# Optimization experiments

Measured on AMD Instinct MI355X. Metric: run time of the kernel, lower is better.

## Reference

```python
import jax, jax.numpy as jnp
import numpy as np

DUNITS = 1024
ATT_DIM = 1024
EPROJ = 1024
T = 16384
SCALING = 2.0


def setup_inputs() -> dict:
    key = jax.random.key(0)
    ks = jax.random.split(key, 8)
    dec_z = jax.random.normal(ks[0], (1, DUNITS), dtype=jnp.float32)
    att_prev = jnp.zeros((1, T), dtype=jnp.float32)
    pre_compute_enc_h = jax.random.normal(ks[1], (1, T, ATT_DIM), dtype=jnp.float32)
    enc_h = jax.random.normal(ks[2], (1, T, EPROJ), dtype=jnp.float32)
    mask = jnp.zeros((1, T), dtype=jnp.float32)
    # learned params: mlp_dec Linear(dunits->att_dim), gvec Linear(att_dim->1)
    W_dec = jax.random.normal(ks[3], (DUNITS, ATT_DIM), dtype=jnp.float32) / np.sqrt(DUNITS)
    b_dec = jnp.zeros((ATT_DIM,), dtype=jnp.float32)
    w_gvec = jax.random.normal(ks[4], (ATT_DIM,), dtype=jnp.float32) / np.sqrt(ATT_DIM)
    b_gvec = jnp.zeros((), dtype=jnp.float32)
    return {
        "dec_z": dec_z,
        "att_prev": att_prev,
        "pre_compute_enc_h": pre_compute_enc_h,
        "enc_h": enc_h,
        "mask": mask,
        "W_dec": W_dec,
        "b_dec": b_dec,
        "w_gvec": w_gvec,
        "b_gvec": b_gvec,
    }


def reference(dec_z, att_prev, pre_compute_enc_h, enc_h, mask, W_dec, b_dec, w_gvec, b_gvec):
    # dec_z: [1, dunits] -> mlp_dec -> [1, 1, att_dim]
    dec_z_tiled = (dec_z @ W_dec + b_dec)[:, None, :]
    # gvec(tanh(pre + tile)).squeeze(2): [1, T]
    e = jnp.einsum("bta,a->bt", jnp.tanh(pre_compute_enc_h + dec_z_tiled), w_gvec) + b_gvec
    e = e + mask
    w = jax.nn.softmax(SCALING * e, axis=1)  # [1, T]
    c = jnp.einsum("bte,bt->be", enc_h, w)   # [1, eproj]
    return (c, w)
```

## Files before the change

### kernel.cpp

```cpp
#include <hip/hip_runtime.h>
#include <math.h>

#define TT   16384
#define ADIM 1024
#define NCH  2048
#define RPB  8
#define NCH2 128

__device__ __forceinline__ float ftanh(float x) {
    float e2 = __expf(2.0f * x);
    return 1.0f - 2.0f * __builtin_amdgcn_rcpf(e2 + 1.0f);
}

__device__ __forceinline__ float pdot(float4 p, float4 d, float4 g) {
    return ftanh(p.x + d.x) * g.x + ftanh(p.y + d.y) * g.y +
           ftanh(p.z + d.z) * g.z + ftanh(p.w + d.w) * g.w;
}

__global__ void k1_gemv_part(const float* __restrict__ z, const float* __restrict__ W,
                             float* __restrict__ part) {
    int b = blockIdx.x, tid = threadIdx.x;
    float4 acc = {0.f, 0.f, 0.f, 0.f};
#pragma unroll
    for (int i = 0; i < 4; ++i) {
        int d = b * 4 + i;
        float zv = z[d];
        float4 w4 = reinterpret_cast<const float4*>(W)[(size_t)d * 256 + tid];
        acc.x += zv * w4.x; acc.y += zv * w4.y; acc.z += zv * w4.z; acc.w += zv * w4.w;
    }
    reinterpret_cast<float4*>(part)[(size_t)b * 256 + tid] = acc;
}

__global__ void k2_gemv_red(const float* __restrict__ part, const float* __restrict__ bdec,
                            float* __restrict__ dp) {
    int b = blockIdx.x, tid = threadIdx.x;
    int lane = tid & 63, wv = tid >> 6;
    int rsub = lane >> 2;
    int colg = lane & 3;
    float4 acc = {0.f, 0.f, 0.f, 0.f};
#pragma unroll
    for (int i = 0; i < 4; ++i) {
        int row = i * 64 + wv * 16 + rsub;
        float4 v = reinterpret_cast<const float4*>(part)[(size_t)row * 256 + b * 4 + colg];
        acc.x += v.x; acc.y += v.y; acc.z += v.z; acc.w += v.w;
    }
#pragma unroll
    for (int off = 4; off <= 32; off <<= 1) {
        acc.x += __shfl_xor(acc.x, off, 64);
        acc.y += __shfl_xor(acc.y, off, 64);
        acc.z += __shfl_xor(acc.z, off, 64);
        acc.w += __shfl_xor(acc.w, off, 64);
    }
    __shared__ float4 lds[4][4];
    if (lane < 4) lds[wv][lane] = acc;
    __syncthreads();
    if (tid < 4) {
        float4 t = {0.f, 0.f, 0.f, 0.f};
#pragma unroll
        for (int w = 0; w < 4; ++w) {
            float4 v = lds[w][tid];
            t.x += v.x; t.y += v.y; t.z += v.z; t.w += v.w;
        }
        float4 bd = reinterpret_cast<const float4*>(bdec)[b * 4 + tid];
        t.x += bd.x; t.y += bd.y; t.z += bd.z; t.w += bd.w;
        reinterpret_cast<float4*>(dp)[b * 4 + tid] = t;
    }
}

__global__ void __launch_bounds__(256) k3_fused(
    const float* __restrict__ pre, const float* __restrict__ enc,
    const float* __restrict__ dp, const float* __restrict__ wg,
    const float* __restrict__ bgp, const float* __restrict__ mask,
    float* __restrict__ e_out, float* __restrict__ m_out,
    float* __restrict__ s_out, float* __restrict__ cpart) {
    int b = blockIdx.x, tid = threadIdx.x;
    int lane = tid & 63, wv = tid >> 6;
    int col = wv * 64 + lane;
    float4 d4 = reinterpret_cast<const float4*>(dp)[col];
    float4 g4 = reinterpret_cast<const float4*>(wg)[col];
    float bgv = bgp[0];
    int t0 = b * RPB;
    const float4* pb = reinterpret_cast<const float4*>(pre) + (size_t)t0 * 256 + col;
    const float4* eb = reinterpret_cast<const float4*>(enc) + (size_t)t0 * 256 + col;

    float4 pv[RPB], ev[RPB];
#pragma unroll
    for (int r = 0; r < RPB; ++r) pv[r] = pb[r * 256];
#pragma unroll
    for (int r = 0; r < RPB; ++r) ev[r] = eb[r * 256];

    float dt[RPB];
#pragma unroll
    for (int r = 0; r < RPB; ++r) dt[r] = pdot(pv[r], d4, g4);
#pragma unroll
    for (int r = 0; r < RPB; ++r) {
#pragma unroll
        for (int off = 32; off; off >>= 1) dt[r] += __shfl_xor(dt[r], off, 64);
    }
    __shared__ float sd[4][RPB];
    if (lane == 0) {
#pragma unroll
        for (int r = 0; r < RPB; ++r) sd[wv][r] = dt[r];
    }
    __syncthreads();
    float et[RPB];
#pragma unroll
    for (int r = 0; r < RPB; ++r)
        et[r] = 2.0f * (sd[0][r] + sd[1][r] + sd[2][r] + sd[3][r] + bgv + mask[t0 + r]);
    if (tid == 0) {
#pragma unroll
        for (int r = 0; r < RPB; ++r) e_out[t0 + r] = et[r];
    }

    float m = et[0];
#pragma unroll
    for (int r = 1; r < RPB; ++r) m = fmaxf(m, et[r]);
    float p[RPB], s = 0.f;
#pragma unroll
    for (int r = 0; r < RPB; ++r) { p[r] = __expf(et[r] - m); s += p[r]; }
    if (tid == 0) { m_out[b] = m; s_out[b] = s; }

    float4 ca = {0.f, 0.f, 0.f, 0.f};
#pragma unroll
    for (int r = 0; r < RPB; ++r) {
        ca.x += p[r] * ev[r].x; ca.y += p[r] * ev[r].y;
        ca.z += p[r] * ev[r].z; ca.w += p[r] * ev[r].w;
    }
    reinterpret_cast<float4*>(cpart)[(size_t)b * 256 + col] = ca;
}

__global__ void __launch_bounds__(256) k4_fold(
    const float* __restrict__ m_arr, const float* __restrict__ s_arr,
    const float* __restrict__ cpart, float* __restrict__ cpart2,
    float* __restrict__ msout) {
    int b = blockIdx.x, tid = threadIdx.x;
    int lane = tid & 63, wv = tid >> 6;
    __shared__ float redm[4], reds[4];
    float mloc = -3.0e38f;
#pragma unroll
    for (int i = 0; i < NCH / 256; ++i) mloc = fmaxf(mloc, m_arr[tid + i * 256]);
#pragma unroll
    for (int off = 32; off; off >>= 1) mloc = fmaxf(mloc, __shfl_xor(mloc, off, 64));
    if (lane == 0) redm[wv] = mloc;
    __syncthreads();
    float M = fmaxf(fmaxf(redm[0], redm[1]), fmaxf(redm[2], redm[3]));
    float4 acc = {0.f, 0.f, 0.f, 0.f};
#pragma unroll
    for (int i = 0; i < NCH / NCH2; ++i) {
        int r = b * (NCH / NCH2) + i;
        float scf = __expf(m_arr[r] - M);
        float4 v = reinterpret_cast<const float4*>(cpart)[(size_t)r * 256 + tid];
        acc.x += scf * v.x; acc.y += scf * v.y; acc.z += scf * v.z; acc.w += scf * v.w;
    }
    reinterpret_cast<float4*>(cpart2)[(size_t)b * 256 + tid] = acc;
    if (b == 0) {
        float sl = 0.f;
#pragma unroll
        for (int i = 0; i < NCH / 256; ++i)
            sl += s_arr[tid + i * 256] * __expf(m_arr[tid + i * 256] - M);
#pragma unroll
        for (int off = 32; off; off >>= 1) sl += __shfl_xor(sl, off, 64);
        if (lane == 0) reds[wv] = sl;
        __syncthreads();
        if (tid == 0) {
            float S = reds[0] + reds[1] + reds[2] + reds[3];
            msout[0] = M;
            msout[1] = 1.0f / S;
        }
    }
}

__global__ void __launch_bounds__(256) k5_final(
    const float* __restrict__ cpart2, const float* __restrict__ e,
    const float* __restrict__ ms, float* __restrict__ c_out,
    float* __restrict__ w_out) {
    int b = blockIdx.x, tid = threadIdx.x;
    float M = ms[0], invS = ms[1];
    if (b < 16) {
        int rs = tid >> 4;
        int cg = tid & 15;
        float4 acc = {0.f, 0.f, 0.f, 0.f};
#pragma unroll
        for (int i = 0; i < NCH2 / 16; ++i) {
            int r = rs * (NCH2 / 16) + i;
            float4 v = reinterpret_cast<const float4*>(cpart2)[(size_t)r * 256 + b * 16 + cg];
            acc.x += v.x; acc.y += v.y; acc.z += v.z; acc.w += v.w;
        }
        __shared__ float4 lds[16][16];
        lds[rs][cg] = acc;
        __syncthreads();
        if (tid < 16) {
            float4 t = {0.f, 0.f, 0.f, 0.f};
#pragma unroll
            for (int r = 0; r < 16; ++r) {
                float4 v = lds[r][tid];
                t.x += v.x; t.y += v.y; t.z += v.z; t.w += v.w;
            }
            t.x *= invS; t.y *= invS; t.z *= invS; t.w *= invS;
            reinterpret_cast<float4*>(c_out)[b * 16 + tid] = t;
        }
    } else {
        int base = (b - 16) * 256 + tid;
        float4 ev = reinterpret_cast<const float4*>(e)[base];
        float4 w;
        w.x = __expf(ev.x - M) * invS;
        w.y = __expf(ev.y - M) * invS;
        w.z = __expf(ev.z - M) * invS;
        w.w = __expf(ev.w - M) * invS;
        reinterpret_cast<float4*>(w_out)[base] = w;
    }
}

extern "C" void kernel_launch(void* const* d_in, const int* in_sizes, int n_in,
                              void* d_out, int out_size, void* d_ws, size_t ws_size,
                              hipStream_t stream) {
    const float* dec_z = (const float*)d_in[0];
    const float* pre   = (const float*)d_in[2];
    const float* enc   = (const float*)d_in[3];
    const float* mask  = (const float*)d_in[4];
    const float* W_dec = (const float*)d_in[5];
    const float* b_dec = (const float*)d_in[6];
    const float* wg    = (const float*)d_in[7];
    const float* bg    = (const float*)d_in[8];

    float* out   = (float*)d_out;
    float* c_out = out;
    float* w_out = out + ADIM;

    float* ws = (float*)d_ws;
    float* part   = ws;
    float* dp     = part + 256 * ADIM;
    float* e_sc   = dp + ADIM;
    float* m_arr  = e_sc + TT;
    float* s_arr  = m_arr + NCH;
    float* cpart  = s_arr + NCH;
    float* cpart2 = cpart + (size_t)NCH * ADIM;
    float* ms     = cpart2 + (size_t)NCH2 * ADIM;

    k1_gemv_part<<<256, 256, 0, stream>>>(dec_z, W_dec, part);
    k2_gemv_red<<<64, 256, 0, stream>>>(part, b_dec, dp);
    k3_fused<<<NCH, 256, 0, stream>>>(pre, enc, dp, wg, bg, mask,
                                      e_sc, m_arr, s_arr, cpart);
    k4_fold<<<NCH2, 256, 0, stream>>>(m_arr, s_arr, cpart, cpart2, ms);
    k5_final<<<32, 256, 0, stream>>>(cpart2, e_sc, ms, c_out, w_out);
}
```

Before: 39.85 us.

## Merge fold and final kernels, double rows per block in main pass

Halves the number of main-kernel blocks by processing 16 rows each and loads rows inline instead of prefetching all of them into registers. The separate fold kernel is removed: the final kernel has every block recompute the global max and sum and directly rescale-reduce all per-chunk partials. This removes one launch and the intermediate partial buffer round-trip. The trade-off is a longer serial reduction over 1024 partials in only 16 blocks and less memory-level parallelism in the main pass.

```diff
diff --git a/kernel.cpp b/kernel.cpp
--- a/kernel.cpp
+++ b/kernel.cpp
@@ -3,9 +3,8 @@
 
 #define TT   16384
 #define ADIM 1024
-#define NCH  2048
-#define RPB  8
-#define NCH2 128
+#define NCH  1024
+#define RPB  16
 
 __device__ __forceinline__ float ftanh(float x) {
     float e2 = __expf(2.0f * x);
@@ -83,15 +82,9 @@
     const float4* pb = reinterpret_cast<const float4*>(pre) + (size_t)t0 * 256 + col;
     const float4* eb = reinterpret_cast<const float4*>(enc) + (size_t)t0 * 256 + col;
 
-    float4 pv[RPB], ev[RPB];
-#pragma unroll
-    for (int r = 0; r < RPB; ++r) pv[r] = pb[r * 256];
-#pragma unroll
-    for (int r = 0; r < RPB; ++r) ev[r] = eb[r * 256];
-
     float dt[RPB];
 #pragma unroll
-    for (int r = 0; r < RPB; ++r) dt[r] = pdot(pv[r], d4, g4);
+    for (int r = 0; r < RPB; ++r) dt[r] = pdot(pb[r * 256], d4, g4);
 #pragma unroll
     for (int r = 0; r < RPB; ++r) {
 #pragma unroll
@@ -123,68 +116,49 @@
     float4 ca = {0.f, 0.f, 0.f, 0.f};
 #pragma unroll
     for (int r = 0; r < RPB; ++r) {
-        ca.x += p[r] * ev[r].x; ca.y += p[r] * ev[r].y;
-        ca.z += p[r] * ev[r].z; ca.w += p[r] * ev[r].w;
+        float4 ev = eb[r * 256];
+        ca.x += p[r] * ev.x; ca.y += p[r] * ev.y;
+        ca.z += p[r] * ev.z; ca.w += p[r] * ev.w;
     }
     reinterpret_cast<float4*>(cpart)[(size_t)b * 256 + col] = ca;
 }
 
-__global__ void __launch_bounds__(256) k4_fold(
+__global__ void __launch_bounds__(256) k4_final(
     const float* __restrict__ m_arr, const float* __restrict__ s_arr,
-    const float* __restrict__ cpart, float* __restrict__ cpart2,
-    float* __restrict__ msout) {
+    const float* __restrict__ cpart, const float* __restrict__ e,
+    float* __restrict__ c_out, float* __restrict__ w_out) {
     int b = blockIdx.x, tid = threadIdx.x;
     int lane = tid & 63, wv = tid >> 6;
     __shared__ float redm[4], reds[4];
-    float mloc = -3.0e38f;
-#pragma unroll
-    for (int i = 0; i < NCH / 256; ++i) mloc = fmaxf(mloc, m_arr[tid + i * 256]);
+    __shared__ float sc[NCH];
+    float4 mv = reinterpret_cast<const float4*>(m_arr)[tid];
+    float mloc = fmaxf(fmaxf(mv.x, mv.y), fmaxf(mv.z, mv.w));
 #pragma unroll
     for (int off = 32; off; off >>= 1) mloc = fmaxf(mloc, __shfl_xor(mloc, off, 64));
     if (lane == 0) redm[wv] = mloc;
     __syncthreads();
     float M = fmaxf(fmaxf(redm[0], redm[1]), fmaxf(redm[2], redm[3]));
-    float4 acc = {0.f, 0.f, 0.f, 0.f};
-#pragma unroll
-    for (int i = 0; i < NCH / NCH2; ++i) {
-        int r = b * (NCH / NCH2) + i;
-        float scf = __expf(m_arr[r] - M);
-        float4 v = reinterpret_cast<const float4*>(cpart)[(size_t)r * 256 + tid];
-        acc.x += scf * v.x; acc.y += scf * v.y; acc.z += scf * v.z; acc.w += scf * v.w;
-    }
-    reinterpret_cast<float4*>(cpart2)[(size_t)b * 256 + tid] = acc;
-    if (b == 0) {
-        float sl = 0.f;
-#pragma unroll
-        for (int i = 0; i < NCH / 256; ++i)
-            sl += s_arr[tid + i * 256] * __expf(m_arr[tid + i * 256] - M);
-#pragma unroll
-        for (int off = 32; off; off >>= 1) sl += __shfl_xor(sl, off, 64);
-        if (lane == 0) reds[wv] = sl;
-        __syncthreads();
-        if (tid == 0) {
-            float S = reds[0] + reds[1] + reds[2] + reds[3];
-            msout[0] = M;
-            msout[1] = 1.0f / S;
-        }
-    }
-}
-
-__global__ void __launch_bounds__(256) k5_final(
-    const float* __restrict__ cpart2, const float* __restrict__ e,
-    const float* __restrict__ ms, float* __restrict__ c_out,
-    float* __restrict__ w_out) {
-    int b = blockIdx.x, tid = threadIdx.x;
-    float M = ms[0], invS = ms[1];
+    float4 sv = reinterpret_cast<const float4*>(s_arr)[tid];
+    float4 scl;
+    scl.x = __expf(mv.x - M); scl.y = __expf(mv.y - M);
+    scl.z = __expf(mv.z - M); scl.w = __expf(mv.w - M);
+    reinterpret_cast<float4*>(sc)[tid] = scl;
+    float sl = sv.x * scl.x + sv.y * scl.y + sv.z * scl.z + sv.w * scl.w;
+#pragma unroll
+    for (int off = 32; off; off >>= 1) sl += __shfl_xor(sl, off, 64);
+    if (lane == 0) reds[wv] = sl;
+    __syncthreads();
+    float invS = 1.0f / (reds[0] + reds[1] + reds[2] + reds[3]);
+
     if (b < 16) {
         int rs = tid >> 4;
         int cg = tid & 15;
         float4 acc = {0.f, 0.f, 0.f, 0.f};
-#pragma unroll
-        for (int i = 0; i < NCH2 / 16; ++i) {
-            int r = rs * (NCH2 / 16) + i;
-            float4 v = reinterpret_cast<const float4*>(cpart2)[(size_t)r * 256 + b * 16 + cg];
-            acc.x += v.x; acc.y += v.y; acc.z += v.z; acc.w += v.w;
+        for (int r = rs; r < NCH; r += 16) {
+            float scf = sc[r];
+            float4 v = reinterpret_cast<const float4*>(cpart)[(size_t)r * 256 + b * 16 + cg];
+            acc.x += scf * v.x; acc.y += scf * v.y;
+            acc.z += scf * v.z; acc.w += scf * v.w;
         }
         __shared__ float4 lds[16][16];
         lds[rs][cg] = acc;
@@ -234,13 +208,10 @@
     float* m_arr  = e_sc + TT;
     float* s_arr  = m_arr + NCH;
     float* cpart  = s_arr + NCH;
-    float* cpart2 = cpart + (size_t)NCH * ADIM;
-    float* ms     = cpart2 + (size_t)NCH2 * ADIM;
 
     k1_gemv_part<<<256, 256, 0, stream>>>(dec_z, W_dec, part);
     k2_gemv_red<<<64, 256, 0, stream>>>(part, b_dec, dp);
     k3_fused<<<NCH, 256, 0, stream>>>(pre, enc, dp, wg, bg, mask,
                                       e_sc, m_arr, s_arr, cpart);
-    k4_fold<<<NCH2, 256, 0, stream>>>(m_arr, s_arr, cpart, cpart2, ms);
-    k5_final<<<32, 256, 0, stream>>>(cpart2, e_sc, ms, c_out, w_out);
-}
+    k4_final<<<32, 256, 0, stream>>>(m_arr, s_arr, cpart, e_sc, c_out, w_out);
+}
```

After: 54.21 us. 1.36x slower.

## Split fused score/context kernel into separate score and context kernels

Applied to the files above, without the earlier changes.

Splits the fused kernel, which read both pre_compute_enc_h and enc_h, into two kernels. One computes the attention scores from pre_compute_enc_h. The other reads those scores back and accumulates the weighted enc_h context. This lowers register pressure per kernel, which may raise occupancy, and lets each pass stream a single tensor. In exchange it adds a kernel launch and a global round-trip for the scores, and it loses the overlap of the two tensor loads within one block.

```diff
diff --git a/kernel.cpp b/kernel.cpp
--- a/kernel.cpp
+++ b/kernel.cpp
@@ -67,12 +67,10 @@
     }
 }
 
-__global__ void __launch_bounds__(256) k3_fused(
-    const float* __restrict__ pre, const float* __restrict__ enc,
-    const float* __restrict__ dp, const float* __restrict__ wg,
-    const float* __restrict__ bgp, const float* __restrict__ mask,
-    float* __restrict__ e_out, float* __restrict__ m_out,
-    float* __restrict__ s_out, float* __restrict__ cpart) {
+__global__ void __launch_bounds__(256) k3a_escore(
+    const float* __restrict__ pre, const float* __restrict__ dp,
+    const float* __restrict__ wg, const float* __restrict__ bgp,
+    const float* __restrict__ mask, float* __restrict__ e_out) {
     int b = blockIdx.x, tid = threadIdx.x;
     int lane = tid & 63, wv = tid >> 6;
     int col = wv * 64 + lane;
@@ -81,17 +79,10 @@
     float bgv = bgp[0];
     int t0 = b * RPB;
     const float4* pb = reinterpret_cast<const float4*>(pre) + (size_t)t0 * 256 + col;
-    const float4* eb = reinterpret_cast<const float4*>(enc) + (size_t)t0 * 256 + col;
-
-    float4 pv[RPB], ev[RPB];
-#pragma unroll
-    for (int r = 0; r < RPB; ++r) pv[r] = pb[r * 256];
-#pragma unroll
-    for (int r = 0; r < RPB; ++r) ev[r] = eb[r * 256];
 
     float dt[RPB];
 #pragma unroll
-    for (int r = 0; r < RPB; ++r) dt[r] = pdot(pv[r], d4, g4);
+    for (int r = 0; r < RPB; ++r) dt[r] = pdot(pb[r * 256], d4, g4);
 #pragma unroll
     for (int r = 0; r < RPB; ++r) {
 #pragma unroll
@@ -103,15 +94,26 @@
         for (int r = 0; r < RPB; ++r) sd[wv][r] = dt[r];
     }
     __syncthreads();
+    if (tid < RPB) {
+        float et = 2.0f * (sd[0][tid] + sd[1][tid] + sd[2][tid] + sd[3][tid]
+                           + bgv + mask[t0 + tid]);
+        e_out[t0 + tid] = et;
+    }
+}
+
+__global__ void __launch_bounds__(256) k3b_ctx(
+    const float* __restrict__ enc, const float* __restrict__ e,
+    float* __restrict__ m_out, float* __restrict__ s_out,
+    float* __restrict__ cpart) {
+    int b = blockIdx.x, tid = threadIdx.x;
+    int lane = tid & 63, wv = tid >> 6;
+    int col = wv * 64 + lane;
+    int t0 = b * RPB;
+    const float4* eb = reinterpret_cast<const float4*>(enc) + (size_t)t0 * 256 + col;
+
     float et[RPB];
 #pragma unroll
-    for (int r = 0; r < RPB; ++r)
-        et[r] = 2.0f * (sd[0][r] + sd[1][r] + sd[2][r] + sd[3][r] + bgv + mask[t0 + r]);
-    if (tid == 0) {
-#pragma unroll
-        for (int r = 0; r < RPB; ++r) e_out[t0 + r] = et[r];
-    }
-
+    for (int r = 0; r < RPB; ++r) et[r] = e[t0 + r];
     float m = et[0];
 #pragma unroll
     for (int r = 1; r < RPB; ++r) m = fmaxf(m, et[r]);
@@ -123,8 +125,9 @@
     float4 ca = {0.f, 0.f, 0.f, 0.f};
 #pragma unroll
     for (int r = 0; r < RPB; ++r) {
-        ca.x += p[r] * ev[r].x; ca.y += p[r] * ev[r].y;
-        ca.z += p[r] * ev[r].z; ca.w += p[r] * ev[r].w;
+        float4 ev = eb[r * 256];
+        ca.x += p[r] * ev.x; ca.y += p[r] * ev.y;
+        ca.z += p[r] * ev.z; ca.w += p[r] * ev.w;
     }
     reinterpret_cast<float4*>(cpart)[(size_t)b * 256 + col] = ca;
 }
@@ -239,8 +242,8 @@
 
     k1_gemv_part<<<256, 256, 0, stream>>>(dec_z, W_dec, part);
     k2_gemv_red<<<64, 256, 0, stream>>>(part, b_dec, dp);
-    k3_fused<<<NCH, 256, 0, stream>>>(pre, enc, dp, wg, bg, mask,
-                                      e_sc, m_arr, s_arr, cpart);
+    k3a_escore<<<NCH, 256, 0, stream>>>(pre, dp, wg, bg, mask, e_sc);
+    k3b_ctx<<<NCH, 256, 0, stream>>>(enc, e_sc, m_arr, s_arr, cpart);
     k4_fold<<<NCH2, 256, 0, stream>>>(m_arr, s_arr, cpart, cpart2, ms);
     k5_final<<<32, 256, 0, stream>>>(cpart2, e_sc, ms, c_out, w_out);
 }
```

After: 42.38 us. +6.3%, slower.
